# Kernel optimization log

Measured on AMD Instinct MI355X. Metric: run time of the kernel, lower is better.

Reference implementation:

```python
import jax, jax.numpy as jnp
import numpy as np

IN_CH = 512
OUT_CH = 512
HEADS = 8
HEAD_DIM = OUT_CH // HEADS
N = 64 * 64  # total flattened tokens


def setup_inputs() -> dict:
    key = jax.random.key(0)
    ks = jax.random.split(key, 10)
    x = jax.random.normal(ks[0], (64, 64, IN_CH), dtype=jnp.float32)
    edge_index = jax.random.randint(ks[1], (2, 65536), 0, N, dtype=jnp.int64)
    # causal temporal mask, broadcastable against scores [N, H, N]
    temporal_mask = jnp.tril(jnp.ones((N, N), dtype=bool))[:, None, :]
    s = 1.0 / np.sqrt(IN_CH)
    Wq = jax.random.uniform(ks[2], (OUT_CH, IN_CH), minval=-s, maxval=s)
    bq = jnp.zeros((OUT_CH,), jnp.float32)
    Wk = jax.random.uniform(ks[3], (OUT_CH, IN_CH), minval=-s, maxval=s)
    bk = jnp.zeros((OUT_CH,), jnp.float32)
    Wv = jax.random.uniform(ks[4], (OUT_CH, IN_CH), minval=-s, maxval=s)
    bv = jnp.zeros((OUT_CH,), jnp.float32)
    Wo = jax.random.uniform(ks[5], (OUT_CH, OUT_CH), minval=-s, maxval=s)
    bo = jnp.zeros((OUT_CH,), jnp.float32)
    return {"x": x, "edge_index": edge_index, "temporal_mask": temporal_mask,
            "Wq": Wq, "bq": bq, "Wk": Wk, "bk": bk, "Wv": Wv, "bv": bv,
            "Wo": Wo, "bo": bo}


def reference(x, edge_index, temporal_mask, Wq, bq, Wk, bk, Wv, bv, Wo, bo):
    # x: [S1, S2, C] -> flatten to [N, C]; edge_index unused (as in source).
    xf = x.reshape(-1, IN_CH)
    q = (xf @ Wq.T + bq).reshape(-1, HEADS, HEAD_DIM)
    k = (xf @ Wk.T + bk).reshape(-1, HEADS, HEAD_DIM)
    v = (xf @ Wv.T + bv).reshape(-1, HEADS, HEAD_DIM)
    scores = jnp.einsum('nhd,mhd->nhm', q, k) / np.sqrt(HEAD_DIM)  # [N,H,N]
    scores = jnp.where(temporal_mask, scores, -jnp.inf)
    attn = jax.nn.softmax(scores, axis=-1)  # dropout omitted (eval mode)
    out = jnp.einsum('nhm,mhd->nhd', attn, v).reshape(-1, OUT_CH)
    return out @ Wo.T + bo  # [N, OUT_CH]
```

## Files before the change

### kernel.cpp

```cpp
#include <hip/hip_runtime.h>
#include <math.h>

#define NT 4096
#define CH 512
#define NHEADS 8
#define HD 64

typedef __attribute__((ext_vector_type(8))) short short8;
typedef __attribute__((ext_vector_type(4))) float f32x4;
typedef unsigned short ushort_t;
typedef unsigned int uint_t;

#define MFMA16 __builtin_amdgcn_mfma_f32_16x16x32_bf16

#define MNEG 1e30f

__device__ __forceinline__ ushort_t f2bf(float x) {
  uint_t u = __float_as_uint(x);
  return (ushort_t)((u + 0x7fffu + ((u >> 16) & 1u)) >> 16);
}
__device__ __forceinline__ float bf2f(ushort_t h) {
  return __uint_as_float(((uint_t)h) << 16);
}

__device__ __forceinline__ void g2l16(const ushort_t* g, ushort_t* l) {
  __builtin_amdgcn_global_load_lds(
      (const __attribute__((address_space(1))) void*)g,
      (__attribute__((address_space(3))) void*)l, 16, 0, 0);
}

__device__ __forceinline__ short8 ldsFrag(const ushort_t* plane, int row, int c4) {
  return *reinterpret_cast<const short8*>(plane + row * 64 + (((c4) ^ (row & 7)) << 3));
}

__global__ __launch_bounds__(256)
void cvt_hi(const float* __restrict__ x,
            const float* __restrict__ Wq, const float* __restrict__ Wk,
            const float* __restrict__ Wv, const float* __restrict__ Wo,
            ushort_t* __restrict__ xh, ushort_t* __restrict__ qh,
            ushort_t* __restrict__ kh, ushort_t* __restrict__ vh,
            ushort_t* __restrict__ oh) {
  const size_t i = ((size_t)blockIdx.x * 256 + threadIdx.x) * 4;
  const float* src;
  ushort_t* dh;
  size_t off;
  if (i < 2097152) { src = x; dh = xh; off = i; }
  else {
    const size_t j = i - 2097152;
    const int wsel = (int)(j >> 18);
    off = j & 262143;
    if (wsel == 0)      { src = Wq; dh = qh; }
    else if (wsel == 1) { src = Wk; dh = kh; }
    else if (wsel == 2) { src = Wv; dh = vh; }
    else                { src = Wo; dh = oh; }
  }
  const float4 v = *reinterpret_cast<const float4*>(src + off);
  const ushort_t hb[4] = {f2bf(v.x), f2bf(v.y), f2bf(v.z), f2bf(v.w)};
  *reinterpret_cast<uint2*>(dh + off) =
      make_uint2((uint_t)hb[0] | ((uint_t)hb[1] << 16), (uint_t)hb[2] | ((uint_t)hb[3] << 16));
}

__device__ __forceinline__ void gemm_hi_core(
    const ushort_t* __restrict__ Ah, const ushort_t* __restrict__ Wh,
    int m0, int n0, int w, int lane, ushort_t* ldsA, ushort_t* ldsW,
    f32x4 acc[2][4]) {
  const int l15 = lane & 15;
  const int g = lane >> 4;
  for (int k0 = 0; k0 < 512; k0 += 64) {
    __syncthreads();
    #pragma unroll
    for (int p = 0; p < 4; ++p) {
      const int c = 256 * p + 64 * w + lane;
      const int r = c >> 3;
      const int sc4 = (c & 7) ^ (r & 7);
      g2l16(Ah + (size_t)(m0 + r) * 512 + k0 + sc4 * 8, &ldsA[(256 * p + 64 * w) * 8]);
    }
    #pragma unroll
    for (int p = 0; p < 2; ++p) {
      const int c = 256 * p + 64 * w + lane;
      const int r = c >> 3;
      const int sc4 = (c & 7) ^ (r & 7);
      g2l16(Wh + (size_t)(n0 + r) * 512 + k0 + sc4 * 8, &ldsW[(256 * p + 64 * w) * 8]);
    }
    __syncthreads();
    #pragma unroll
    for (int s = 0; s < 2; ++s) {
      short8 ah[2];
      #pragma unroll
      for (int mt = 0; mt < 2; ++mt)
        ah[mt] = ldsFrag(ldsA, 32 * w + 16 * mt + l15, 4 * s + g);
      #pragma unroll
      for (int nt = 0; nt < 4; ++nt) {
        const short8 wh = ldsFrag(ldsW, 16 * nt + l15, 4 * s + g);
        #pragma unroll
        for (int mt = 0; mt < 2; ++mt)
          acc[mt][nt] = MFMA16(ah[mt], wh, acc[mt][nt], 0, 0, 0);
      }
    }
  }
}

__global__ __launch_bounds__(256)
void gemm_qkv_bf16(const ushort_t* __restrict__ xh,
                   const ushort_t* __restrict__ Wqh, const float* __restrict__ bq,
                   const ushort_t* __restrict__ Wkh, const float* __restrict__ bk,
                   const ushort_t* __restrict__ Wvh, const float* __restrict__ bv,
                   ushort_t* __restrict__ Qhi, ushort_t* __restrict__ Khi,
                   ushort_t* __restrict__ Vthi) {
  __shared__ ushort_t ldsA[128 * 64];
  __shared__ ushort_t ldsW[64 * 64];
  const int z = blockIdx.z;
  const ushort_t* Wh = (z == 0) ? Wqh : (z == 1) ? Wkh : Wvh;
  const float* bias = (z == 0) ? bq : (z == 1) ? bk : bv;

  const int t = threadIdx.x;
  const int w = t >> 6;
  const int lane = t & 63;
  const int l15 = lane & 15;
  const int g = lane >> 4;
  const int m0 = blockIdx.x * 128;
  const int n0 = blockIdx.y * 64;

  f32x4 acc[2][4];
  #pragma unroll
  for (int mt = 0; mt < 2; ++mt)
    #pragma unroll
    for (int nt = 0; nt < 4; ++nt) acc[mt][nt] = f32x4{0.f, 0.f, 0.f, 0.f};

  gemm_hi_core(xh, Wh, m0, n0, w, lane, ldsA, ldsW, acc);

  if (z < 2) {
    ushort_t* Hi = z ? Khi : Qhi;
    const float sc = z ? 1.0f : 0.125f;
    #pragma unroll
    for (int mt = 0; mt < 2; ++mt) {
      const int mb = m0 + 32 * w + 16 * mt + 4 * g;
      #pragma unroll
      for (int nt = 0; nt < 4; ++nt) {
        const int col = n0 + 16 * nt + l15;
        const float bv_ = bias[col];
        #pragma unroll
        for (int r = 0; r < 4; ++r)
          Hi[(size_t)(mb + r) * 512 + col] = f2bf((acc[mt][nt][r] + bv_) * sc);
      }
    }
  } else {
    #pragma unroll
    for (int mt = 0; mt < 2; ++mt) {
      const int mb = m0 + 32 * w + 16 * mt + 4 * g;
      #pragma unroll
      for (int nt = 0; nt < 4; ++nt) {
        const int n = n0 + 16 * nt + l15;
        const float bv_ = bias[n];
        ushort_t hb[4];
        #pragma unroll
        for (int r = 0; r < 4; ++r) hb[r] = f2bf(acc[mt][nt][r] + bv_);
        *reinterpret_cast<uint2*>(&Vthi[(size_t)n * 4096 + mb]) =
            make_uint2((uint_t)hb[0] | ((uint_t)hb[1] << 16),
                       (uint_t)hb[2] | ((uint_t)hb[3] << 16));
      }
    }
  }
}

__global__ __launch_bounds__(256)
void gemm_out_bf16(const ushort_t* __restrict__ Ahi, const ushort_t* __restrict__ Woh,
                   const float* __restrict__ bias, float* __restrict__ C) {
  __shared__ ushort_t ldsA[128 * 64];
  __shared__ ushort_t ldsW[64 * 64];
  const int t = threadIdx.x;
  const int w = t >> 6;
  const int lane = t & 63;
  const int l15 = lane & 15;
  const int g = lane >> 4;
  const int m0 = blockIdx.x * 128;
  const int n0 = blockIdx.y * 64;

  f32x4 acc[2][4];
  #pragma unroll
  for (int mt = 0; mt < 2; ++mt)
    #pragma unroll
    for (int nt = 0; nt < 4; ++nt) acc[mt][nt] = f32x4{0.f, 0.f, 0.f, 0.f};

  gemm_hi_core(Ahi, Woh, m0, n0, w, lane, ldsA, ldsW, acc);

  #pragma unroll
  for (int mt = 0; mt < 2; ++mt) {
    const int mb = m0 + 32 * w + 16 * mt + 4 * g;
    #pragma unroll
    for (int nt = 0; nt < 4; ++nt) {
      const int col = n0 + 16 * nt + l15;
      const float bv_ = bias[col];
      #pragma unroll
      for (int r = 0; r < 4; ++r)
        C[(size_t)(mb + r) * 512 + col] = acc[mt][nt][r] + bv_;
    }
  }
}

__global__ __launch_bounds__(512)
void attn_mfma(const ushort_t* __restrict__ Qhi, const ushort_t* __restrict__ Khi,
               const ushort_t* __restrict__ Vthi,
               ushort_t* __restrict__ Opart, float2* __restrict__ MLpart) {
  __shared__ ushort_t ldsK[2][64 * 64];
  __shared__ ushort_t ldsV[2][64 * 64];
  __shared__ ushort_t ldsP[8][16 * 64];

  const int t = threadIdx.x;
  const int h = blockIdx.y;
  const int w = t >> 6;
  const int lane = t & 63;
  const int l15 = lane & 15;
  const int g = lane >> 4;

  const int bx = blockIdx.x;
  const int qb = 31 - bx / 3;
  const int sp = bx - 3 * (bx / 3);
  const int ntp = qb + 1;
  const int len = (ntp + 2) / 3;
  const int pb0 = sp * len;
  const int pb1e = (pb0 + len < ntp) ? (pb0 + len) : ntp;
  const int q0 = qb * 128;
  const int qr = q0 + w * 16 + l15;

  const short8 ones = {(short)0x3F80, (short)0x3F80, (short)0x3F80, (short)0x3F80,
                       (short)0x3F80, (short)0x3F80, (short)0x3F80, (short)0x3F80};

  short8 qh[2];
  #pragma unroll
  for (int s = 0; s < 2; ++s)
    qh[s] = *reinterpret_cast<const short8*>(
        Qhi + (size_t)qr * 512 + h * 64 + 32 * s + 8 * g);

  float mrun[4], lrun[4];
  f32x4 accO[4];
  #pragma unroll
  for (int r = 0; r < 4; ++r) { mrun[r] = -MNEG; lrun[r] = 0.f; }
  #pragma unroll
  for (int dt = 0; dt < 4; ++dt) accO[dt] = f32x4{0.f, 0.f, 0.f, 0.f};

  for (int pair = pb0; pair < pb1e; ++pair) {
    __syncthreads();
    {
      const int c = w * 64 + lane;
      const int r = c >> 3;
      const int sc4 = (c & 7) ^ (r & 7);
      const int ldst = (w * 64) * 8;
      const int kt0 = 2 * pair, kt1 = 2 * pair + 1;
      g2l16(Khi + (size_t)(kt0 * 64 + r) * 512 + h * 64 + sc4 * 8, &ldsK[0][ldst]);
      g2l16(Khi + (size_t)(kt1 * 64 + r) * 512 + h * 64 + sc4 * 8, &ldsK[1][ldst]);
      g2l16(Vthi + (size_t)(h * 64 + r) * 4096 + kt0 * 64 + sc4 * 8, &ldsV[0][ldst]);
      g2l16(Vthi + (size_t)(h * 64 + r) * 4096 + kt1 * 64 + sc4 * 8, &ldsV[1][ldst]);
    }
    __syncthreads();

    #pragma unroll
    for (int st = 0; st < 2; ++st) {
      const int kt = 2 * pair + st;

      f32x4 accS[4];
      #pragma unroll
      for (int nt = 0; nt < 4; ++nt) accS[nt] = f32x4{0.f, 0.f, 0.f, 0.f};
      __builtin_amdgcn_s_setprio(1);
      #pragma unroll
      for (int s = 0; s < 2; ++s) {
        #pragma unroll
        for (int nt = 0; nt < 4; ++nt) {
          const short8 kh = ldsFrag(ldsK[st], 16 * nt + l15, 4 * s + g);
          accS[nt] = MFMA16(qh[s], kh, accS[nt], 0, 0, 0);
        }
      }
      __builtin_amdgcn_s_setprio(0);

      if (pair == qb) {
        #pragma unroll
        for (int nt = 0; nt < 4; ++nt) {
          const int kg = kt * 64 + 16 * nt + l15;
          #pragma unroll
          for (int r = 0; r < 4; ++r) {
            const int qg = q0 + w * 16 + 4 * g + r;
            if (kg > qg) accS[nt][r] = -INFINITY;
          }
        }
      }

      float pmax[4];
      #pragma unroll
      for (int r = 0; r < 4; ++r)
        pmax[r] = fmaxf(fmaxf(accS[0][r], accS[1][r]), fmaxf(accS[2][r], accS[3][r]));
      float dd = pmax[0] - mrun[0];
      #pragma unroll
      for (int r = 1; r < 4; ++r) dd = fmaxf(dd, pmax[r] - mrun[r]);
      if (!__all(dd <= 8.0f)) {
        #pragma unroll
        for (int off = 1; off < 16; off <<= 1)
          #pragma unroll
          for (int r = 0; r < 4; ++r) pmax[r] = fmaxf(pmax[r], __shfl_xor(pmax[r], off));
        #pragma unroll
        for (int r = 0; r < 4; ++r) {
          const float mn = fmaxf(mrun[r], pmax[r]);
          const float al = __expf(mrun[r] - mn);
          mrun[r] = mn;
          lrun[r] *= al;
          #pragma unroll
          for (int dt = 0; dt < 4; ++dt) accO[dt][r] *= al;
        }
      }
      #pragma unroll
      for (int nt = 0; nt < 4; ++nt)
        #pragma unroll
        for (int r = 0; r < 4; ++r) {
          const float p = __expf(accS[nt][r] - mrun[r]);
          const int row = 4 * g + r;
          ldsP[w][row * 64 + (((2 * nt + (l15 >> 3)) ^ (row & 7)) << 3) + (l15 & 7)]
              = f2bf(p);
        }
      short8 pah[2];
      #pragma unroll
      for (int s = 0; s < 2; ++s) pah[s] = ldsFrag(ldsP[w], l15, 4 * s + g);

      f32x4 accL = f32x4{0.f, 0.f, 0.f, 0.f};
      __builtin_amdgcn_s_setprio(1);
      #pragma unroll
      for (int s = 0; s < 2; ++s) {
        accL = MFMA16(pah[s], ones, accL, 0, 0, 0);
        #pragma unroll
        for (int dt = 0; dt < 4; ++dt) {
          const short8 vh = ldsFrag(ldsV[st], 16 * dt + l15, 4 * s + g);
          accO[dt] = MFMA16(pah[s], vh, accO[dt], 0, 0, 0);
        }
      }
      __builtin_amdgcn_s_setprio(0);
      #pragma unroll
      for (int r = 0; r < 4; ++r) lrun[r] += accL[r];
    }
  }

  #pragma unroll
  for (int r = 0; r < 4; ++r) {
    const int rw = w * 16 + 4 * g + r;
    const size_t pbase = ((((size_t)sp * 32 + qb) * 8 + h) * 128 + rw) * 64;
    #pragma unroll
    for (int dt = 0; dt < 4; ++dt)
      Opart[pbase + 16 * dt + l15] = f2bf(accO[dt][r]);
    if (l15 == 0)
      MLpart[(((size_t)sp * 32 + qb) * 8 + h) * 128 + rw] = make_float2(mrun[r], lrun[r]);
  }
}

__global__ __launch_bounds__(512)
void attn_combine(const ushort_t* __restrict__ Opart, const float2* __restrict__ MLpart,
                  ushort_t* __restrict__ Ahi) {
  const int qb = blockIdx.x;
  const int h = blockIdx.y;
  const int t = threadIdx.x;
  const int row = t >> 2;
  const int c0 = (t & 3) * 16;
  const size_t mlidx = (((size_t)qb) * 8 + h) * 128 + row;
  const size_t SPS = (size_t)32 * 8 * 128;
  const float2 ml0 = MLpart[mlidx];
  const float2 ml1 = MLpart[mlidx + SPS];
  const float2 ml2 = MLpart[mlidx + 2 * SPS];
  const float M = fmaxf(fmaxf(ml0.x, ml1.x), ml2.x);
  const float w0 = __expf(ml0.x - M);
  const float w1 = __expf(ml1.x - M);
  const float w2 = __expf(ml2.x - M);
  const float inv = 1.0f / (w0 * ml0.y + w1 * ml1.y + w2 * ml2.y);
  const size_t b0 = mlidx * 64;
  const size_t b1 = (mlidx + SPS) * 64;
  const size_t b2 = (mlidx + 2 * SPS) * 64;
  #pragma unroll
  for (int p = 0; p < 4; ++p) {
    const int col = c0 + p * 4;
    const uint2 u0 = *reinterpret_cast<const uint2*>(&Opart[b0 + col]);
    const uint2 u1 = *reinterpret_cast<const uint2*>(&Opart[b1 + col]);
    const uint2 u2 = *reinterpret_cast<const uint2*>(&Opart[b2 + col]);
    float f[4];
    f[0] = bf2f((ushort_t)(u0.x & 0xffff)) * w0 + bf2f((ushort_t)(u1.x & 0xffff)) * w1
         + bf2f((ushort_t)(u2.x & 0xffff)) * w2;
    f[1] = bf2f((ushort_t)(u0.x >> 16)) * w0 + bf2f((ushort_t)(u1.x >> 16)) * w1
         + bf2f((ushort_t)(u2.x >> 16)) * w2;
    f[2] = bf2f((ushort_t)(u0.y & 0xffff)) * w0 + bf2f((ushort_t)(u1.y & 0xffff)) * w1
         + bf2f((ushort_t)(u2.y & 0xffff)) * w2;
    f[3] = bf2f((ushort_t)(u0.y >> 16)) * w0 + bf2f((ushort_t)(u1.y >> 16)) * w1
         + bf2f((ushort_t)(u2.y >> 16)) * w2;
    ushort_t hb[4];
    #pragma unroll
    for (int j = 0; j < 4; ++j) hb[j] = f2bf(f[j] * inv);
    const size_t idx = (size_t)(qb * 128 + row) * 512 + h * 64 + col;
    *reinterpret_cast<uint2*>(&Ahi[idx]) =
        make_uint2((uint_t)hb[0] | ((uint_t)hb[1] << 16), (uint_t)hb[2] | ((uint_t)hb[3] << 16));
  }
}

extern "C" void kernel_launch(void* const* d_in, const int* in_sizes, int n_in,
                              void* d_out, int out_size, void* d_ws, size_t ws_size,
                              hipStream_t stream) {
  const float* x  = (const float*)d_in[0];
  const float* Wq = (const float*)d_in[3];
  const float* bq = (const float*)d_in[4];
  const float* Wk = (const float*)d_in[5];
  const float* bk = (const float*)d_in[6];
  const float* Wv = (const float*)d_in[7];
  const float* bv = (const float*)d_in[8];
  const float* Wo = (const float*)d_in[9];
  const float* bo = (const float*)d_in[10];
  float* out = (float*)d_out;

  ushort_t* p = (ushort_t*)d_ws;
  const size_t NC = (size_t)NT * CH;
  const size_t WW = (size_t)CH * CH;
  ushort_t* xhi = p;            p += NC;
  ushort_t* Wqh = p;            p += WW;
  ushort_t* Wkh = p;            p += WW;
  ushort_t* Wvh = p;            p += WW;
  ushort_t* Woh = p;            p += WW;
  ushort_t* Qhi = p;            p += NC;
  ushort_t* Khi = p;            p += NC;
  ushort_t* Vthi = p;           p += NC;
  ushort_t* Ahi = p;            p += NC;
  ushort_t* Opart = p;          p += (size_t)3 * 32 * 8 * 128 * 64;
  float2* MLpart = (float2*)p;

  cvt_hi<<<3072, 256, 0, stream>>>(x, Wq, Wk, Wv, Wo, xhi, Wqh, Wkh, Wvh, Woh);
  gemm_qkv_bf16<<<dim3(32, 8, 3), 256, 0, stream>>>(
      xhi, Wqh, bq, Wkh, bk, Wvh, bv, Qhi, Khi, Vthi);
  attn_mfma<<<dim3(96, 8), 512, 0, stream>>>(Qhi, Khi, Vthi, Opart, MLpart);
  attn_combine<<<dim3(32, 8), 512, 0, stream>>>(Opart, MLpart, Ahi);
  gemm_out_bf16<<<dim3(32, 8), 256, 0, stream>>>(Ahi, Woh, bo, out);
}
```

Measured before the change: 88.74 us.

## Compute transposed S tile and pass P to PV MFMA via register permutes

The QK^T MFMA now computes the transposed score tile (K as A operand), so each lane holds one query row's scores. Row max and sum reduce within the lane, plus two cross-lane shuffles, and running max and sum become scalars per lane. The P matrix is repacked into the MFMA A-operand layout with ds_bpermute instead of a round trip through an LDS staging buffer, and the extra ones-MFMA used for the row sum is removed. In exchange the kernel issues many bpermute operations and needs extra permutes to broadcast the rescale factors to the output accumulator rows.

```diff
diff --git a/kernel.cpp b/kernel.cpp
--- a/kernel.cpp
+++ b/kernel.cpp
@@ -204,7 +204,6 @@
                ushort_t* __restrict__ Opart, float2* __restrict__ MLpart) {
   __shared__ ushort_t ldsK[2][64 * 64];
   __shared__ ushort_t ldsV[2][64 * 64];
-  __shared__ ushort_t ldsP[8][16 * 64];
 
   const int t = threadIdx.x;
   const int h = blockIdx.y;
@@ -223,21 +222,20 @@
   const int q0 = qb * 128;
   const int qr = q0 + w * 16 + l15;
 
-  const short8 ones = {(short)0x3F80, (short)0x3F80, (short)0x3F80, (short)0x3F80,
-                       (short)0x3F80, (short)0x3F80, (short)0x3F80, (short)0x3F80};
-
   short8 qh[2];
   #pragma unroll
   for (int s = 0; s < 2; ++s)
     qh[s] = *reinterpret_cast<const short8*>(
         Qhi + (size_t)qr * 512 + h * 64 + 32 * s + 8 * g);
 
-  float mrun[4], lrun[4];
+  float mrun = -MNEG, lrun = 0.f;
   f32x4 accO[4];
   #pragma unroll
-  for (int r = 0; r < 4; ++r) { mrun[r] = -MNEG; lrun[r] = 0.f; }
-  #pragma unroll
   for (int dt = 0; dt < 4; ++dt) accO[dt] = f32x4{0.f, 0.f, 0.f, 0.f};
+
+  const int idxA = 4 * (l15 + 32 * (g & 1));
+  const int idxB = idxA + 64;
+  const bool hiSel = (g >> 1) != 0;
 
   for (int pair = pb0; pair < pb1e; ++pair) {
     __syncthreads();
@@ -258,81 +256,109 @@
     for (int st = 0; st < 2; ++st) {
       const int kt = 2 * pair + st;
 
-      f32x4 accS[4];
-      #pragma unroll
-      for (int nt = 0; nt < 4; ++nt) accS[nt] = f32x4{0.f, 0.f, 0.f, 0.f};
+      f32x4 accT[4];
+      #pragma unroll
+      for (int ntk = 0; ntk < 4; ++ntk) accT[ntk] = f32x4{0.f, 0.f, 0.f, 0.f};
       __builtin_amdgcn_s_setprio(1);
       #pragma unroll
       for (int s = 0; s < 2; ++s) {
         #pragma unroll
-        for (int nt = 0; nt < 4; ++nt) {
-          const short8 kh = ldsFrag(ldsK[st], 16 * nt + l15, 4 * s + g);
-          accS[nt] = MFMA16(qh[s], kh, accS[nt], 0, 0, 0);
+        for (int ntk = 0; ntk < 4; ++ntk) {
+          const short8 kh = ldsFrag(ldsK[st], 16 * ntk + l15, 4 * s + g);
+          accT[ntk] = MFMA16(kh, qh[s], accT[ntk], 0, 0, 0);
         }
       }
       __builtin_amdgcn_s_setprio(0);
 
       if (pair == qb) {
         #pragma unroll
-        for (int nt = 0; nt < 4; ++nt) {
-          const int kg = kt * 64 + 16 * nt + l15;
+        for (int ntk = 0; ntk < 4; ++ntk) {
           #pragma unroll
           for (int r = 0; r < 4; ++r) {
-            const int qg = q0 + w * 16 + 4 * g + r;
-            if (kg > qg) accS[nt][r] = -INFINITY;
+            const int kg = kt * 64 + 16 * ntk + 4 * g + r;
+            if (kg > qr) accT[ntk][r] = -INFINITY;
           }
         }
       }
 
-      float pmax[4];
-      #pragma unroll
-      for (int r = 0; r < 4; ++r)
-        pmax[r] = fmaxf(fmaxf(accS[0][r], accS[1][r]), fmaxf(accS[2][r], accS[3][r]));
-      float dd = pmax[0] - mrun[0];
-      #pragma unroll
-      for (int r = 1; r < 4; ++r) dd = fmaxf(dd, pmax[r] - mrun[r]);
-      if (!__all(dd <= 8.0f)) {
-        #pragma unroll
-        for (int off = 1; off < 16; off <<= 1)
+      float pmax = accT[0][0];
+      #pragma unroll
+      for (int ntk = 0; ntk < 4; ++ntk)
+        #pragma unroll
+        for (int r = 0; r < 4; ++r) pmax = fmaxf(pmax, accT[ntk][r]);
+      if (!__all(pmax - mrun <= 8.0f)) {
+        float pm = fmaxf(pmax, __shfl_xor(pmax, 16));
+        pm = fmaxf(pm, __shfl_xor(pm, 32));
+        const float mn = fmaxf(mrun, pm);
+        const float al = __expf(mrun - mn);
+        mrun = mn;
+        lrun *= al;
+        #pragma unroll
+        for (int r = 0; r < 4; ++r) {
+          const float alr = __int_as_float(
+              __builtin_amdgcn_ds_bpermute(4 * (4 * g + r), __float_as_int(al)));
           #pragma unroll
-          for (int r = 0; r < 4; ++r) pmax[r] = fmaxf(pmax[r], __shfl_xor(pmax[r], off));
+          for (int dt = 0; dt < 4; ++dt) accO[dt][r] *= alr;
+        }
+      }
+      float psum = 0.f;
+      uint_t pk[4][2];
+      #pragma unroll
+      for (int ntk = 0; ntk < 4; ++ntk) {
+        ushort_t b[4];
         #pragma unroll
         for (int r = 0; r < 4; ++r) {
-          const float mn = fmaxf(mrun[r], pmax[r]);
-          const float al = __expf(mrun[r] - mn);
-          mrun[r] = mn;
-          lrun[r] *= al;
-          #pragma unroll
-          for (int dt = 0; dt < 4; ++dt) accO[dt][r] *= al;
+          const float p = __expf(accT[ntk][r] - mrun);
+          b[r] = f2bf(p);
+          psum += bf2f(b[r]);
         }
-      }
-      #pragma unroll
-      for (int nt = 0; nt < 4; ++nt)
-        #pragma unroll
-        for (int r = 0; r < 4; ++r) {
-          const float p = __expf(accS[nt][r] - mrun[r]);
-          const int row = 4 * g + r;
-          ldsP[w][row * 64 + (((2 * nt + (l15 >> 3)) ^ (row & 7)) << 3) + (l15 & 7)]
-              = f2bf(p);
-        }
-      short8 pah[2];
-      #pragma unroll
-      for (int s = 0; s < 2; ++s) pah[s] = ldsFrag(ldsP[w], l15, 4 * s + g);
-
-      f32x4 accL = f32x4{0.f, 0.f, 0.f, 0.f};
+        pk[ntk][0] = (uint_t)b[0] | ((uint_t)b[1] << 16);
+        pk[ntk][1] = (uint_t)b[2] | ((uint_t)b[3] << 16);
+      }
+      psum += __shfl_xor(psum, 16);
+      psum += __shfl_xor(psum, 32);
+      lrun += psum;
+
+      union { uint_t u[4]; short8 s8; } pa0, pa1;
+      {
+        const int a00 = __builtin_amdgcn_ds_bpermute(idxA, (int)pk[0][0]);
+        const int a01 = __builtin_amdgcn_ds_bpermute(idxA, (int)pk[0][1]);
+        const int b00 = __builtin_amdgcn_ds_bpermute(idxB, (int)pk[0][0]);
+        const int b01 = __builtin_amdgcn_ds_bpermute(idxB, (int)pk[0][1]);
+        const int a10 = __builtin_amdgcn_ds_bpermute(idxA, (int)pk[1][0]);
+        const int a11 = __builtin_amdgcn_ds_bpermute(idxA, (int)pk[1][1]);
+        const int b10 = __builtin_amdgcn_ds_bpermute(idxB, (int)pk[1][0]);
+        const int b11 = __builtin_amdgcn_ds_bpermute(idxB, (int)pk[1][1]);
+        pa0.u[0] = (uint_t)(hiSel ? a10 : a00);
+        pa0.u[1] = (uint_t)(hiSel ? a11 : a01);
+        pa0.u[2] = (uint_t)(hiSel ? b10 : b00);
+        pa0.u[3] = (uint_t)(hiSel ? b11 : b01);
+        const int a20 = __builtin_amdgcn_ds_bpermute(idxA, (int)pk[2][0]);
+        const int a21 = __builtin_amdgcn_ds_bpermute(idxA, (int)pk[2][1]);
+        const int b20 = __builtin_amdgcn_ds_bpermute(idxB, (int)pk[2][0]);
+        const int b21 = __builtin_amdgcn_ds_bpermute(idxB, (int)pk[2][1]);
+        const int a30 = __builtin_amdgcn_ds_bpermute(idxA, (int)pk[3][0]);
+        const int a31 = __builtin_amdgcn_ds_bpermute(idxA, (int)pk[3][1]);
+        const int b30 = __builtin_amdgcn_ds_bpermute(idxB, (int)pk[3][0]);
+        const int b31 = __builtin_amdgcn_ds_bpermute(idxB, (int)pk[3][1]);
+        pa1.u[0] = (uint_t)(hiSel ? a30 : a20);
+        pa1.u[1] = (uint_t)(hiSel ? a31 : a21);
+        pa1.u[2] = (uint_t)(hiSel ? b30 : b20);
+        pa1.u[3] = (uint_t)(hiSel ? b31 : b21);
+      }
+
       __builtin_amdgcn_s_setprio(1);
       #pragma unroll
-      for (int s = 0; s < 2; ++s) {
-        accL = MFMA16(pah[s], ones, accL, 0, 0, 0);
-        #pragma unroll
-        for (int dt = 0; dt < 4; ++dt) {
-          const short8 vh = ldsFrag(ldsV[st], 16 * dt + l15, 4 * s + g);
-          accO[dt] = MFMA16(pah[s], vh, accO[dt], 0, 0, 0);
-        }
+      for (int dt = 0; dt < 4; ++dt) {
+        const short8 vh = ldsFrag(ldsV[st], 16 * dt + l15, g);
+        accO[dt] = MFMA16(pa0.s8, vh, accO[dt], 0, 0, 0);
+      }
+      #pragma unroll
+      for (int dt = 0; dt < 4; ++dt) {
+        const short8 vh = ldsFrag(ldsV[st], 16 * dt + l15, 4 + g);
+        accO[dt] = MFMA16(pa1.s8, vh, accO[dt], 0, 0, 0);
       }
       __builtin_amdgcn_s_setprio(0);
-      #pragma unroll
-      for (int r = 0; r < 4; ++r) lrun[r] += accL[r];
     }
   }
 
@@ -343,9 +369,10 @@
     #pragma unroll
     for (int dt = 0; dt < 4; ++dt)
       Opart[pbase + 16 * dt + l15] = f2bf(accO[dt][r]);
-    if (l15 == 0)
-      MLpart[(((size_t)sp * 32 + qb) * 8 + h) * 128 + rw] = make_float2(mrun[r], lrun[r]);
-  }
+  }
+  if (g == 0)
+    MLpart[(((size_t)sp * 32 + qb) * 8 + h) * 128 + w * 16 + l15] =
+        make_float2(mrun, lrun);
 }
 
 __global__ __launch_bounds__(512)
```

New measurement: 95.08 us. 1.07x slower.

## Fuse split-K attention combine into output projection GEMM A-tile loading

Applied to the files above, without the earlier changes.

Removes the separate attn_combine kernel and the Ahi intermediate buffer. The output GEMM now builds its A tile directly in LDS by merging the three attention partials with their max/sum statistics for each head's K-slice. This saves one launch and the global write and read of the combined activations. In exchange, the merge runs redundantly in each of the 8 N-column blocks, and the A-side loads become synchronous register loads instead of the async g2l16 path.

```diff
diff --git a/kernel.cpp b/kernel.cpp
--- a/kernel.cpp
+++ b/kernel.cpp
@@ -163,41 +163,6 @@
   }
 }
 
-__global__ __launch_bounds__(256)
-void gemm_out_bf16(const ushort_t* __restrict__ Ahi, const ushort_t* __restrict__ Woh,
-                   const float* __restrict__ bias, float* __restrict__ C) {
-  __shared__ ushort_t ldsA[128 * 64];
-  __shared__ ushort_t ldsW[64 * 64];
-  const int t = threadIdx.x;
-  const int w = t >> 6;
-  const int lane = t & 63;
-  const int l15 = lane & 15;
-  const int g = lane >> 4;
-  const int m0 = blockIdx.x * 128;
-  const int n0 = blockIdx.y * 64;
-
-  f32x4 acc[2][4];
-  #pragma unroll
-  for (int mt = 0; mt < 2; ++mt)
-    #pragma unroll
-    for (int nt = 0; nt < 4; ++nt) acc[mt][nt] = f32x4{0.f, 0.f, 0.f, 0.f};
-
-  gemm_hi_core(Ahi, Woh, m0, n0, w, lane, ldsA, ldsW, acc);
-
-  #pragma unroll
-  for (int mt = 0; mt < 2; ++mt) {
-    const int mb = m0 + 32 * w + 16 * mt + 4 * g;
-    #pragma unroll
-    for (int nt = 0; nt < 4; ++nt) {
-      const int col = n0 + 16 * nt + l15;
-      const float bv_ = bias[col];
-      #pragma unroll
-      for (int r = 0; r < 4; ++r)
-        C[(size_t)(mb + r) * 512 + col] = acc[mt][nt][r] + bv_;
-    }
-  }
-}
-
 __global__ __launch_bounds__(512)
 void attn_mfma(const ushort_t* __restrict__ Qhi, const ushort_t* __restrict__ Khi,
                const ushort_t* __restrict__ Vthi,
@@ -348,48 +313,102 @@
   }
 }
 
-__global__ __launch_bounds__(512)
-void attn_combine(const ushort_t* __restrict__ Opart, const float2* __restrict__ MLpart,
-                  ushort_t* __restrict__ Ahi) {
+__global__ __launch_bounds__(256)
+void gemm_out_fused(const ushort_t* __restrict__ Opart,
+                    const float2* __restrict__ MLpart,
+                    const ushort_t* __restrict__ Woh,
+                    const float* __restrict__ bias, float* __restrict__ C) {
+  __shared__ ushort_t ldsA[128 * 64];
+  __shared__ ushort_t ldsW[64 * 64];
+  const int t = threadIdx.x;
+  const int w = t >> 6;
+  const int lane = t & 63;
+  const int l15 = lane & 15;
+  const int g = lane >> 4;
   const int qb = blockIdx.x;
-  const int h = blockIdx.y;
-  const int t = threadIdx.x;
-  const int row = t >> 2;
-  const int c0 = (t & 3) * 16;
-  const size_t mlidx = (((size_t)qb) * 8 + h) * 128 + row;
+  const int m0 = qb * 128;
+  const int n0 = blockIdx.y * 64;
   const size_t SPS = (size_t)32 * 8 * 128;
-  const float2 ml0 = MLpart[mlidx];
-  const float2 ml1 = MLpart[mlidx + SPS];
-  const float2 ml2 = MLpart[mlidx + 2 * SPS];
-  const float M = fmaxf(fmaxf(ml0.x, ml1.x), ml2.x);
-  const float w0 = __expf(ml0.x - M);
-  const float w1 = __expf(ml1.x - M);
-  const float w2 = __expf(ml2.x - M);
-  const float inv = 1.0f / (w0 * ml0.y + w1 * ml1.y + w2 * ml2.y);
-  const size_t b0 = mlidx * 64;
-  const size_t b1 = (mlidx + SPS) * 64;
-  const size_t b2 = (mlidx + 2 * SPS) * 64;
-  #pragma unroll
-  for (int p = 0; p < 4; ++p) {
-    const int col = c0 + p * 4;
-    const uint2 u0 = *reinterpret_cast<const uint2*>(&Opart[b0 + col]);
-    const uint2 u1 = *reinterpret_cast<const uint2*>(&Opart[b1 + col]);
-    const uint2 u2 = *reinterpret_cast<const uint2*>(&Opart[b2 + col]);
-    float f[4];
-    f[0] = bf2f((ushort_t)(u0.x & 0xffff)) * w0 + bf2f((ushort_t)(u1.x & 0xffff)) * w1
-         + bf2f((ushort_t)(u2.x & 0xffff)) * w2;
-    f[1] = bf2f((ushort_t)(u0.x >> 16)) * w0 + bf2f((ushort_t)(u1.x >> 16)) * w1
-         + bf2f((ushort_t)(u2.x >> 16)) * w2;
-    f[2] = bf2f((ushort_t)(u0.y & 0xffff)) * w0 + bf2f((ushort_t)(u1.y & 0xffff)) * w1
-         + bf2f((ushort_t)(u2.y & 0xffff)) * w2;
-    f[3] = bf2f((ushort_t)(u0.y >> 16)) * w0 + bf2f((ushort_t)(u1.y >> 16)) * w1
-         + bf2f((ushort_t)(u2.y >> 16)) * w2;
-    ushort_t hb[4];
-    #pragma unroll
-    for (int j = 0; j < 4; ++j) hb[j] = f2bf(f[j] * inv);
-    const size_t idx = (size_t)(qb * 128 + row) * 512 + h * 64 + col;
-    *reinterpret_cast<uint2*>(&Ahi[idx]) =
-        make_uint2((uint_t)hb[0] | ((uint_t)hb[1] << 16), (uint_t)hb[2] | ((uint_t)hb[3] << 16));
+
+  f32x4 acc[2][4];
+  #pragma unroll
+  for (int mt = 0; mt < 2; ++mt)
+    #pragma unroll
+    for (int nt = 0; nt < 4; ++nt) acc[mt][nt] = f32x4{0.f, 0.f, 0.f, 0.f};
+
+  for (int k0 = 0; k0 < 512; k0 += 64) {
+    const int hh = k0 >> 6;
+    __syncthreads();
+    #pragma unroll
+    for (int p = 0; p < 2; ++p) {
+      const int c = 256 * p + 64 * w + lane;
+      const int r = c >> 3;
+      const int sc4 = (c & 7) ^ (r & 7);
+      g2l16(Woh + (size_t)(n0 + r) * 512 + k0 + sc4 * 8, &ldsW[(256 * p + 64 * w) * 8]);
+    }
+    #pragma unroll
+    for (int p = 0; p < 4; ++p) {
+      const int c = 256 * p + 64 * w + lane;
+      const int r = c >> 3;
+      const int c4 = c & 7;
+      const size_t mlidx = (((size_t)qb) * 8 + hh) * 128 + r;
+      const float2 ml0 = MLpart[mlidx];
+      const float2 ml1 = MLpart[mlidx + SPS];
+      const float2 ml2 = MLpart[mlidx + 2 * SPS];
+      const float M = fmaxf(fmaxf(ml0.x, ml1.x), ml2.x);
+      const float w0 = __expf(ml0.x - M);
+      const float w1 = __expf(ml1.x - M);
+      const float w2 = __expf(ml2.x - M);
+      const float inv = 1.0f / (w0 * ml0.y + w1 * ml1.y + w2 * ml2.y);
+      const size_t ob = mlidx * 64 + c4 * 8;
+      const uint4 u0 = *reinterpret_cast<const uint4*>(&Opart[ob]);
+      const uint4 u1 = *reinterpret_cast<const uint4*>(&Opart[ob + SPS * 64]);
+      const uint4 u2 = *reinterpret_cast<const uint4*>(&Opart[ob + 2 * SPS * 64]);
+      const uint_t a0[4] = {u0.x, u0.y, u0.z, u0.w};
+      const uint_t a1[4] = {u1.x, u1.y, u1.z, u1.w};
+      const uint_t a2[4] = {u2.x, u2.y, u2.z, u2.w};
+      uint_t out[4];
+      #pragma unroll
+      for (int j = 0; j < 4; ++j) {
+        const float flo = (bf2f((ushort_t)(a0[j] & 0xffff)) * w0 +
+                           bf2f((ushort_t)(a1[j] & 0xffff)) * w1 +
+                           bf2f((ushort_t)(a2[j] & 0xffff)) * w2) * inv;
+        const float fhi = (bf2f((ushort_t)(a0[j] >> 16)) * w0 +
+                           bf2f((ushort_t)(a1[j] >> 16)) * w1 +
+                           bf2f((ushort_t)(a2[j] >> 16)) * w2) * inv;
+        out[j] = (uint_t)f2bf(flo) | ((uint_t)f2bf(fhi) << 16);
+      }
+      *reinterpret_cast<uint4*>(&ldsA[r * 64 + ((c4 ^ (r & 7)) << 3)]) =
+          make_uint4(out[0], out[1], out[2], out[3]);
+    }
+    __syncthreads();
+    #pragma unroll
+    for (int s = 0; s < 2; ++s) {
+      short8 ah[2];
+      #pragma unroll
+      for (int mt = 0; mt < 2; ++mt)
+        ah[mt] = ldsFrag(ldsA, 32 * w + 16 * mt + l15, 4 * s + g);
+      #pragma unroll
+      for (int nt = 0; nt < 4; ++nt) {
+        const short8 wh = ldsFrag(ldsW, 16 * nt + l15, 4 * s + g);
+        #pragma unroll
+        for (int mt = 0; mt < 2; ++mt)
+          acc[mt][nt] = MFMA16(ah[mt], wh, acc[mt][nt], 0, 0, 0);
+      }
+    }
+  }
+
+  #pragma unroll
+  for (int mt = 0; mt < 2; ++mt) {
+    const int mb = m0 + 32 * w + 16 * mt + 4 * g;
+    #pragma unroll
+    for (int nt = 0; nt < 4; ++nt) {
+      const int col = n0 + 16 * nt + l15;
+      const float bv_ = bias[col];
+      #pragma unroll
+      for (int r = 0; r < 4; ++r)
+        C[(size_t)(mb + r) * 512 + col] = acc[mt][nt][r] + bv_;
+    }
   }
 }
 
@@ -418,7 +437,6 @@
   ushort_t* Qhi = p;            p += NC;
   ushort_t* Khi = p;            p += NC;
   ushort_t* Vthi = p;           p += NC;
-  ushort_t* Ahi = p;            p += NC;
   ushort_t* Opart = p;          p += (size_t)3 * 32 * 8 * 128 * 64;
   float2* MLpart = (float2*)p;
 
@@ -426,6 +444,5 @@
   gemm_qkv_bf16<<<dim3(32, 8, 3), 256, 0, stream>>>(
       xhi, Wqh, bq, Wkh, bk, Wvh, bv, Qhi, Khi, Vthi);
   attn_mfma<<<dim3(96, 8), 512, 0, stream>>>(Qhi, Khi, Vthi, Opart, MLpart);
-  attn_combine<<<dim3(32, 8), 512, 0, stream>>>(Opart, MLpart, Ahi);
-  gemm_out_bf16<<<dim3(32, 8), 256, 0, stream>>>(Ahi, Woh, bo, out);
-}
+  gemm_out_fused<<<dim3(32, 8), 256, 0, stream>>>(Opart, MLpart, Woh, bo, out);
+}
```

Measured after the change: 108.6 us. 22.4% more time.
